# Kernel tuning notes

Hardware: AMD Instinct MI355X
Metric: run time of the kernel (lower is better)

Reference implementation:

```python
import jax, jax.numpy as jnp
import numpy as np

N_NODES = 50000
N_EDGES = 800000
D_FEAT = 64


def setup_inputs() -> dict:
    key = jax.random.key(0)
    k1, k2, k3, k4 = jax.random.split(key, 4)
    rows = jnp.sort(jax.random.randint(k1, (N_EDGES,), 0, N_NODES, dtype=jnp.int64))
    cols = jax.random.randint(k2, (N_EDGES,), 0, N_NODES, dtype=jnp.int64)
    vals = jax.random.uniform(k3, (N_EDGES,), dtype=jnp.float32)
    embeds = jax.random.normal(k4, (N_NODES, D_FEAT), dtype=jnp.float32)
    return {"rows": rows, "cols": cols, "vals": vals, "embeds": embeds}


def reference(rows, cols, vals, embeds):
    # torch.spmm(adj, embeds) with adj in COO form:
    # out[r] = sum_{e: rows[e]==r} vals[e] * embeds[cols[e]]
    gathered = vals[:, None] * embeds[cols]            # [E, D]
    out = jax.ops.segment_sum(gathered, rows, num_segments=N_NODES)  # [N, D]
    return out
```

## Files before the change

kernel.cpp:

```cpp
#include <hip/hip_runtime.h>


#define D_FEAT 64
#define BLOCK 256

__global__ __launch_bounds__(256) void build_row_ptr(
    const int* __restrict__ rows, int* __restrict__ row_ptr,
    int n_nodes, int n_edges)
{
    int r = blockIdx.x * blockDim.x + threadIdx.x;
    if (r > n_nodes) return;
    int lo = 0, hi = n_edges;
    while (lo < hi) {
        int mid = (lo + hi) >> 1;
        if (rows[mid] < r) lo = mid + 1; else hi = mid;
    }
    row_ptr[r] = lo;
}

__global__ __launch_bounds__(BLOCK) void spmm_wave_per_row(
    const int* __restrict__ row_ptr,
    const int* __restrict__ cols,
    const float* __restrict__ vals,
    const float* __restrict__ embeds,
    float* __restrict__ out,
    int n_nodes)
{
    const int wave = (int)((blockIdx.x * (unsigned)BLOCK + threadIdx.x) >> 6);
    const int lane = (int)(threadIdx.x & 63u);
    if (wave >= n_nodes) return;

    const int s = row_ptr[wave];
    const int t = row_ptr[wave + 1];

    float a0 = 0.f, a1 = 0.f, a2 = 0.f, a3 = 0.f;
    int e = s;
    for (; e + 4 <= t; e += 4) {
        const int   c0 = cols[e],     c1 = cols[e + 1];
        const int   c2 = cols[e + 2], c3 = cols[e + 3];
        const float v0 = vals[e],     v1 = vals[e + 1];
        const float v2 = vals[e + 2], v3 = vals[e + 3];
        const float x0 = embeds[(size_t)c0 * D_FEAT + lane];
        const float x1 = embeds[(size_t)c1 * D_FEAT + lane];
        const float x2 = embeds[(size_t)c2 * D_FEAT + lane];
        const float x3 = embeds[(size_t)c3 * D_FEAT + lane];
        a0 = fmaf(v0, x0, a0);
        a1 = fmaf(v1, x1, a1);
        a2 = fmaf(v2, x2, a2);
        a3 = fmaf(v3, x3, a3);
    }
    for (; e < t; ++e)
        a0 = fmaf(vals[e], embeds[(size_t)cols[e] * D_FEAT + lane], a0);

    out[(size_t)wave * D_FEAT + lane] = (a0 + a1) + (a2 + a3);
}

extern "C" void kernel_launch(void* const* d_in, const int* in_sizes, int n_in,
                              void* d_out, int out_size, void* d_ws, size_t ws_size,
                              hipStream_t stream) {
    const int*   rows   = (const int*)d_in[0];
    const int*   cols   = (const int*)d_in[1];
    const float* vals   = (const float*)d_in[2];
    const float* embeds = (const float*)d_in[3];
    float*       out    = (float*)d_out;

    const int n_edges = in_sizes[0];
    const int n_nodes = out_size / D_FEAT;

    int* row_ptr = (int*)d_ws;

    {
        const int nthreads = n_nodes + 1;
        const int nblocks = (nthreads + 255) / 256;
        build_row_ptr<<<nblocks, 256, 0, stream>>>(rows, row_ptr, n_nodes, n_edges);
    }
    {
        const int waves_per_block = BLOCK / 64;
        const int nblocks = (n_nodes + waves_per_block - 1) / waves_per_block;
        spmm_wave_per_row<<<nblocks, BLOCK, 0, stream>>>(row_ptr, cols, vals, embeds,
                                                         out, n_nodes);
    }
}
```

Before: 113.3 us.

## Vectorize SpMM gathers with float4 sub-wave edges and edge-parallel row_ptr build

The SpMM kernel now splits each 64-lane wave into four 16-lane groups. Each group loads a full embedding row as float4, so four edges are processed in parallel, and the partial sums are combined with xor shuffles. This widens memory transactions and raises the number of edges in flight per wave, at the cost of a cross-lane reduction and a masked tail. The row_ptr construction also changes from a per-node binary search to a per-edge boundary scan that writes offsets directly.

```diff
diff --git a/kernel.cpp b/kernel.cpp
--- a/kernel.cpp
+++ b/kernel.cpp
@@ -4,21 +4,20 @@
 #define D_FEAT 64
 #define BLOCK 256
 
-__global__ __launch_bounds__(256) void build_row_ptr(
+__global__ __launch_bounds__(BLOCK) void build_row_ptr_edges(
     const int* __restrict__ rows, int* __restrict__ row_ptr,
     int n_nodes, int n_edges)
 {
-    int r = blockIdx.x * blockDim.x + threadIdx.x;
-    if (r > n_nodes) return;
-    int lo = 0, hi = n_edges;
-    while (lo < hi) {
-        int mid = (lo + hi) >> 1;
-        if (rows[mid] < r) lo = mid + 1; else hi = mid;
-    }
-    row_ptr[r] = lo;
+    const int e = blockIdx.x * BLOCK + threadIdx.x;
+    if (e >= n_edges) return;
+    const int r  = rows[e];
+    const int rp = (e == 0) ? -1 : rows[e - 1];
+    for (int v = rp + 1; v <= r; ++v) row_ptr[v] = e;
+    if (e == n_edges - 1)
+        for (int v = r + 1; v <= n_nodes; ++v) row_ptr[v] = n_edges;
 }
 
-__global__ __launch_bounds__(BLOCK) void spmm_wave_per_row(
+__global__ __launch_bounds__(BLOCK) void spmm_row_f4(
     const int* __restrict__ row_ptr,
     const int* __restrict__ cols,
     const float* __restrict__ vals,
@@ -27,32 +26,51 @@
     int n_nodes)
 {
     const int wave = (int)((blockIdx.x * (unsigned)BLOCK + threadIdx.x) >> 6);
+    if (wave >= n_nodes) return;
     const int lane = (int)(threadIdx.x & 63u);
-    if (wave >= n_nodes) return;
+    const int sub  = lane >> 4;
+    const int f4   = lane & 15;
 
     const int s = row_ptr[wave];
     const int t = row_ptr[wave + 1];
 
-    float a0 = 0.f, a1 = 0.f, a2 = 0.f, a3 = 0.f;
+    float4 acc = make_float4(0.f, 0.f, 0.f, 0.f);
+
     int e = s;
-    for (; e + 4 <= t; e += 4) {
-        const int   c0 = cols[e],     c1 = cols[e + 1];
-        const int   c2 = cols[e + 2], c3 = cols[e + 3];
-        const float v0 = vals[e],     v1 = vals[e + 1];
-        const float v2 = vals[e + 2], v3 = vals[e + 3];
-        const float x0 = embeds[(size_t)c0 * D_FEAT + lane];
-        const float x1 = embeds[(size_t)c1 * D_FEAT + lane];
-        const float x2 = embeds[(size_t)c2 * D_FEAT + lane];
-        const float x3 = embeds[(size_t)c3 * D_FEAT + lane];
-        a0 = fmaf(v0, x0, a0);
-        a1 = fmaf(v1, x1, a1);
-        a2 = fmaf(v2, x2, a2);
-        a3 = fmaf(v3, x3, a3);
+    for (; e + 8 <= t; e += 8) {
+        const int i0 = e + sub;
+        const int i1 = e + 4 + sub;
+        const int   c0 = cols[i0], c1 = cols[i1];
+        const float v0 = vals[i0], v1 = vals[i1];
+        const float4 x0 = ((const float4*)(embeds + (size_t)c0 * D_FEAT))[f4];
+        const float4 x1 = ((const float4*)(embeds + (size_t)c1 * D_FEAT))[f4];
+        acc.x = fmaf(v0, x0.x, acc.x); acc.y = fmaf(v0, x0.y, acc.y);
+        acc.z = fmaf(v0, x0.z, acc.z); acc.w = fmaf(v0, x0.w, acc.w);
+        acc.x = fmaf(v1, x1.x, acc.x); acc.y = fmaf(v1, x1.y, acc.y);
+        acc.z = fmaf(v1, x1.z, acc.z); acc.w = fmaf(v1, x1.w, acc.w);
     }
-    for (; e < t; ++e)
-        a0 = fmaf(vals[e], embeds[(size_t)cols[e] * D_FEAT + lane], a0);
+    for (; e < t; e += 4) {
+        const int me  = e + sub;
+        const int idx = (me < t) ? me : (t - 1);
+        float v = vals[idx];
+        if (me >= t) v = 0.f;
+        const int c = cols[idx];
+        const float4 x = ((const float4*)(embeds + (size_t)c * D_FEAT))[f4];
+        acc.x = fmaf(v, x.x, acc.x); acc.y = fmaf(v, x.y, acc.y);
+        acc.z = fmaf(v, x.z, acc.z); acc.w = fmaf(v, x.w, acc.w);
+    }
 
-    out[(size_t)wave * D_FEAT + lane] = (a0 + a1) + (a2 + a3);
+    acc.x += __shfl_xor(acc.x, 16, 64);
+    acc.y += __shfl_xor(acc.y, 16, 64);
+    acc.z += __shfl_xor(acc.z, 16, 64);
+    acc.w += __shfl_xor(acc.w, 16, 64);
+    acc.x += __shfl_xor(acc.x, 32, 64);
+    acc.y += __shfl_xor(acc.y, 32, 64);
+    acc.z += __shfl_xor(acc.z, 32, 64);
+    acc.w += __shfl_xor(acc.w, 32, 64);
+
+    if (lane < 16)
+        ((float4*)(out + (size_t)wave * D_FEAT))[f4] = acc;
 }
 
 extern "C" void kernel_launch(void* const* d_in, const int* in_sizes, int n_in,
@@ -70,14 +88,12 @@
     int* row_ptr = (int*)d_ws;
 
     {
-        const int nthreads = n_nodes + 1;
-        const int nblocks = (nthreads + 255) / 256;
-        build_row_ptr<<<nblocks, 256, 0, stream>>>(rows, row_ptr, n_nodes, n_edges);
+        const int nblocks = (n_edges + BLOCK - 1) / BLOCK;
+        build_row_ptr_edges<<<nblocks, BLOCK, 0, stream>>>(rows, row_ptr, n_nodes, n_edges);
     }
     {
         const int waves_per_block = BLOCK / 64;
         const int nblocks = (n_nodes + waves_per_block - 1) / waves_per_block;
-        spmm_wave_per_row<<<nblocks, BLOCK, 0, stream>>>(row_ptr, cols, vals, embeds,
-                                                         out, n_nodes);
+        spmm_row_f4<<<nblocks, BLOCK, 0, stream>>>(row_ptr, cols, vals, embeds, out, n_nodes);
     }
 }
```

Measured after the change: 100.8 us. 11.0% less time.
